# Kernel optimization log

Measured on AMD Instinct MI355X. Metric: run time of the kernel, lower is better.

The kernel has to match this reference:

```python
import jax, jax.numpy as jnp
import numpy as np

D_MODEL = 1024
N_HEADS = 16
HEAD_DIM = D_MODEL // N_HEADS
FFN_DIM = 4096
T = 2048
LN_EPS = 1e-5


def layer_norm(x, g, b):
    mu = jnp.mean(x, axis=-1, keepdims=True)
    var = jnp.mean(jnp.square(x - mu), axis=-1, keepdims=True)
    return (x - mu) * jax.lax.rsqrt(var + LN_EPS) * g + b


def setup_inputs() -> dict:
    key = jax.random.key(0)
    ks = jax.random.split(key, 12)
    s = 0.02
    x = jax.random.normal(ks[0], (1, T, D_MODEL), dtype=jnp.float32)
    # causal mask: True means masked (strict upper triangle)
    causal_mask = jnp.triu(jnp.ones((T, T), dtype=bool), k=1)
    # ALiBi bias: -slope * distance, per head
    slopes = 2.0 ** (-8.0 * (jnp.arange(1, N_HEADS + 1, dtype=jnp.float32) / N_HEADS))
    pos = jnp.arange(T, dtype=jnp.float32)
    dist = pos[None, :] - pos[:, None]  # (T, T)
    alibi_bias = slopes[:, None, None] * jnp.minimum(dist, 0.0)[None]  # (H, T, T)
    inp = {
        "x": x,
        "causal_mask": causal_mask,
        "alibi_bias": alibi_bias.astype(jnp.float32),
        "wq": jax.random.normal(ks[1], (D_MODEL, D_MODEL), jnp.float32) * s,
        "bq": jnp.zeros((D_MODEL,), jnp.float32),
        "wk": jax.random.normal(ks[2], (D_MODEL, D_MODEL), jnp.float32) * s,
        "bk": jnp.zeros((D_MODEL,), jnp.float32),
        "wv": jax.random.normal(ks[3], (D_MODEL, D_MODEL), jnp.float32) * s,
        "bv": jnp.zeros((D_MODEL,), jnp.float32),
        "wo": jax.random.normal(ks[4], (D_MODEL, D_MODEL), jnp.float32) * s,
        "bo": jnp.zeros((D_MODEL,), jnp.float32),
        "w1": jax.random.normal(ks[5], (D_MODEL, FFN_DIM), jnp.float32) * s,
        "b1": jnp.zeros((FFN_DIM,), jnp.float32),
        "w2": jax.random.normal(ks[6], (FFN_DIM, D_MODEL), jnp.float32) * s,
        "b2": jnp.zeros((D_MODEL,), jnp.float32),
        "g1": jnp.ones((D_MODEL,), jnp.float32),
        "be1": jnp.zeros((D_MODEL,), jnp.float32),
        "g2": jnp.ones((D_MODEL,), jnp.float32),
        "be2": jnp.zeros((D_MODEL,), jnp.float32),
    }
    return inp


def reference(x, causal_mask, alibi_bias, wq, bq, wk, bk, wv, bv, wo, bo,
              w1, b1, w2, b2, g1, be1, g2, be2):
    B, Tt, D = x.shape
    H, hd = N_HEADS, HEAD_DIM
    x_norm = layer_norm(x, g1, be1)
    # projections -> (B, H, T, hd)
    def split_heads(y):
        return y.reshape(B, Tt, H, hd).transpose(0, 2, 1, 3)
    Q = split_heads(x_norm @ wq + bq)
    K = split_heads(x_norm @ wk + bk)
    V = split_heads(x_norm @ wv + bv)
    scale = jnp.sqrt(jnp.float32(hd))
    scores = jnp.einsum('bhqd,bhkd->bhqk', Q, K) / scale
    scores = scores + alibi_bias[None]
    scores = jnp.where(causal_mask[None, None], -jnp.inf, scores)
    attn = jax.nn.softmax(scores, axis=-1)
    attn_out = jnp.einsum('bhqk,bhkd->bhqd', attn, V)
    attn_out = attn_out.transpose(0, 2, 1, 3).reshape(B, Tt, D)
    attn_out = attn_out @ wo + bo
    x = x + attn_out
    x_norm = layer_norm(x, g2, be2)
    h = jax.nn.gelu(x_norm @ w1 + b1, approximate=False)
    ffn_out = h @ w2 + b2
    return x + ffn_out
```

## Files before the change

kernel.cpp:

```cpp
#include <hip/hip_runtime.h>
#include <hip/hip_bf16.h>
#include <math.h>

#define T_SEQ 2048
#define D_MODEL 1024
#define N_HEADS 16
#define HEAD_DIM 64
#define FFN_DIM 4096

typedef _Float16 halfx8 __attribute__((ext_vector_type(8)));
typedef _Float16 halfx4 __attribute__((ext_vector_type(4)));
typedef float floatx4 __attribute__((ext_vector_type(4)));

__device__ __forceinline__ void async_ld16(const _Float16* g, _Float16* l) {
  __builtin_amdgcn_global_load_lds(
      (const __attribute__((address_space(1))) unsigned int*)g,
      (__attribute__((address_space(3))) unsigned int*)l, 16, 0, 0);
}

template <int N> __device__ __forceinline__ void wait_barrier();
template <> __device__ __forceinline__ void wait_barrier<3>() {
  asm volatile("s_waitcnt vmcnt(3)\n\ts_barrier" ::: "memory");
}
template <> __device__ __forceinline__ void wait_barrier<4>() {
  asm volatile("s_waitcnt vmcnt(4)\n\ts_barrier" ::: "memory");
}

__global__ __launch_bounds__(256) void ln_h_kernel(
    const float* __restrict__ x, const float* __restrict__ g,
    const float* __restrict__ b, _Float16* __restrict__ y) {
  int row = blockIdx.x;
  const float* xr = x + (size_t)row * D_MODEL;
  _Float16* yr = y + (size_t)row * D_MODEL;
  int tid = threadIdx.x;
  int lid = tid & 63, wid = tid >> 6;
  __shared__ float red[8];

  float4 v = *(const float4*)&xr[tid * 4];
  float sum = v.x + v.y + v.z + v.w;
  for (int o = 32; o > 0; o >>= 1) sum += __shfl_down(sum, o, 64);
  if (lid == 0) red[wid] = sum;
  __syncthreads();
  if (tid == 0) { float t = 0; for (int i = 0; i < 4; i++) t += red[i]; red[0] = t; }
  __syncthreads();
  float mu = red[0] * (1.0f / D_MODEL);
  __syncthreads();

  float dx = v.x - mu, dy = v.y - mu, dz = v.z - mu, dw = v.w - mu;
  float vs = dx * dx + dy * dy + dz * dz + dw * dw;
  for (int o = 32; o > 0; o >>= 1) vs += __shfl_down(vs, o, 64);
  if (lid == 0) red[wid] = vs;
  __syncthreads();
  if (tid == 0) { float t = 0; for (int i = 0; i < 4; i++) t += red[i]; red[0] = t; }
  __syncthreads();
  float rstd = rsqrtf(red[0] * (1.0f / D_MODEL) + 1e-5f);

  float4 gv = *(const float4*)&g[tid * 4];
  float4 bv = *(const float4*)&b[tid * 4];
  halfx4 o;
  o[0] = (_Float16)(dx * rstd * gv.x + bv.x);
  o[1] = (_Float16)(dy * rstd * gv.y + bv.y);
  o[2] = (_Float16)(dz * rstd * gv.z + bv.z);
  o[3] = (_Float16)(dw * rstd * gv.w + bv.w);
  *(halfx4*)&yr[tid * 4] = o;
}

__global__ __launch_bounds__(256) void prep_kernel(
    const float* __restrict__ wq, const float* __restrict__ wk,
    const float* __restrict__ wv, const float* __restrict__ wo,
    const float* __restrict__ w1, const float* __restrict__ w2,
    const float* __restrict__ bq, const float* __restrict__ bk,
    const float* __restrict__ bv, _Float16* __restrict__ Wqkvt,
    _Float16* __restrict__ Wot, _Float16* __restrict__ W1t,
    _Float16* __restrict__ W2t, float* __restrict__ bqkv) {
  int bId = blockIdx.x;
  int tid = threadIdx.x;
  if (bId >= 12288) {
    int i = (bId - 12288) * 256 + tid;
    if (i < 1024) bqkv[i] = bq[i];
    else if (i < 2048) bqkv[i] = bk[i - 1024];
    else bqkv[i] = bv[i - 2048];
    return;
  }
  const float* in; _Float16* outp; int K, N, t;
  if (bId < 1024)      { in = wq; outp = Wqkvt;                 K = 1024; N = 1024; t = bId; }
  else if (bId < 2048) { in = wk; outp = Wqkvt + 1024 * 1024;   K = 1024; N = 1024; t = bId - 1024; }
  else if (bId < 3072) { in = wv; outp = Wqkvt + 2 * 1024 * 1024; K = 1024; N = 1024; t = bId - 2048; }
  else if (bId < 4096) { in = wo; outp = Wot;                   K = 1024; N = 1024; t = bId - 3072; }
  else if (bId < 8192) { in = w1; outp = W1t;                   K = 1024; N = 4096; t = bId - 4096; }
  else                 { in = w2; outp = W2t;                   K = 4096; N = 1024; t = bId - 8192; }
  int ntn = N / 32;
  int tk = (t / ntn) * 32, tn = (t % ntn) * 32;

  __shared__ float tile[32][33];
  int r = tid >> 3, c = (tid & 7) * 4;
  float4 v = *(const float4*)&in[(size_t)(tk + r) * N + tn + c];
  tile[r][c] = v.x; tile[r][c + 1] = v.y; tile[r][c + 2] = v.z; tile[r][c + 3] = v.w;
  __syncthreads();
  halfx4 o;
  o[0] = (_Float16)tile[c][r];
  o[1] = (_Float16)tile[c + 1][r];
  o[2] = (_Float16)tile[c + 2][r];
  o[3] = (_Float16)tile[c + 3][r];
  *(halfx4*)&outp[(size_t)(tn + r) * K + tk + c] = o;
}

template <int MODE, int BM, int BN>
__global__ __launch_bounds__(256) void hgemm_kernel(
    const _Float16* __restrict__ A, const _Float16* __restrict__ Bt,
    const float* __restrict__ bias, const float* __restrict__ res,
    float* __restrict__ Cf, _Float16* __restrict__ Ch,
    _Float16* __restrict__ Vtg, int M, int N, int K) {
  constexpr int TM = BM / 32;
  constexpr int TN = BN / 32;
  constexpr int AR = BM / 64;
  constexpr int BR = BN / 64;
  constexpr int L = AR + BR;
  __shared__ _Float16 As[3][BM][32];
  __shared__ _Float16 Bs[3][BN][32];
  const int tid = threadIdx.x;
  const int w = tid >> 6, lane = tid & 63;
  const int l16 = lane & 15, quad = lane >> 4;
  const int m0 = blockIdx.y * BM, n0 = blockIdx.x * BN;
  const int wm = (w >> 1) * (BM / 2), wn = (w & 1) * (BN / 2);

  floatx4 acc[TM][TN];
#pragma unroll
  for (int i = 0; i < TM; i++)
#pragma unroll
    for (int j = 0; j < TN; j++) acc[i][j] = (floatx4){0.f, 0.f, 0.f, 0.f};

  const int srow = w * 16 + (lane >> 2);
  const int gg = (lane & 3) ^ ((srow >> 1) & 3);
  const _Float16* Agp = A + (size_t)(m0 + srow) * K + gg * 8;
  const _Float16* Bgp = Bt + (size_t)(n0 + srow) * K + gg * 8;

  const int colA = (quad ^ ((l16 >> 1) & 3)) * 8;

  const int NIT = K / 32;
#define HG_ISSUE(buf, k0)                                                     \
  {                                                                           \
    _Pragma("unroll") for (int i = 0; i < AR; i++)                            \
        async_ld16(Agp + (k0) + (size_t)i * 64 * K, &As[buf][i * 64 + w * 16][0]); \
    _Pragma("unroll") for (int i = 0; i < BR; i++)                            \
        async_ld16(Bgp + (k0) + (size_t)i * 64 * K, &Bs[buf][i * 64 + w * 16][0]); \
  }
  HG_ISSUE(0, 0)
  if (NIT > 1) HG_ISSUE(1, 32)

  for (int it = 0; it < NIT; it++) {
    const int buf = it % 3;
    wait_barrier<L>();
    if (it + 2 < NIT) HG_ISSUE((it + 2) % 3, (it + 2) * 32)
    halfx8 af[TM], bf[TN];
#pragma unroll
    for (int mt = 0; mt < TM; mt++)
      af[mt] = *(const halfx8*)&As[buf][wm + mt * 16 + l16][colA];
#pragma unroll
    for (int nt = 0; nt < TN; nt++)
      bf[nt] = *(const halfx8*)&Bs[buf][wn + nt * 16 + l16][colA];
#pragma unroll
    for (int mt = 0; mt < TM; mt++)
#pragma unroll
      for (int nt = 0; nt < TN; nt++)
        acc[mt][nt] = __builtin_amdgcn_mfma_f32_16x16x32_f16(af[mt], bf[nt], acc[mt][nt], 0, 0, 0);
  }

#pragma unroll
  for (int mt = 0; mt < TM; mt++) {
    int row0 = m0 + wm + mt * 16 + quad * 4;
#pragma unroll
    for (int nt = 0; nt < TN; nt++) {
      int col = n0 + wn + nt * 16 + l16;
      float bv = bias[col];
      float vv[4];
#pragma unroll
      for (int r = 0; r < 4; r++) {
        float v = acc[mt][nt][r] + bv;
        if (MODE == 1) v = 0.5f * v * (1.0f + erff(v * 0.70710678118f));
        vv[r] = v;
      }
      if (MODE == 2) {
#pragma unroll
        for (int r = 0; r < 4; r++)
          Cf[(size_t)(row0 + r) * N + col] = vv[r] + res[(size_t)(row0 + r) * N + col];
      } else if (MODE == 3) {
        if (col < 2048) {
#pragma unroll
          for (int r = 0; r < 4; r++)
            Ch[(size_t)(row0 + r) * 2048 + col] = (_Float16)vv[r];
        } else {
          halfx4 pk;
#pragma unroll
          for (int r = 0; r < 4; r++) pk[r] = (_Float16)vv[r];
          *(halfx4*)&Vtg[(size_t)(col - 2048) * T_SEQ + row0] = pk;
        }
      } else {
#pragma unroll
        for (int r = 0; r < 4; r++)
          Ch[(size_t)(row0 + r) * N + col] = (_Float16)vv[r];
      }
    }
  }
}

#define LROW 72
__global__ __launch_bounds__(256) void flash_attn_kernel(
    const _Float16* __restrict__ QK, const _Float16* __restrict__ Vtg,
    _Float16* __restrict__ out) {
  __shared__ _Float16 Ks[3][64][64];
  __shared__ _Float16 Vt[3][64][64];
  __shared__ _Float16 Ps[4][16][LROW];

  const int h = blockIdx.y;
  const int qt = 31 - blockIdx.x;
  const int q0 = qt * 64;
  const int tid = threadIdx.x;
  const int w = tid >> 6;
  const int lane = tid & 63;
  const int l16 = lane & 15;
  const int quad = lane >> 4;

  const _Float16* Qg = QK + h * HEAD_DIM;
  const _Float16* Kg = QK + 1024 + h * HEAD_DIM;
  const _Float16* Vg = Vtg + (size_t)h * HEAD_DIM * T_SEQ;

  const _Float16* qp = Qg + (size_t)(q0 + w * 16 + l16) * 2048;
  halfx8 qa0 = *(const halfx8*)(qp + quad * 8);
  halfx8 qa1 = *(const halfx8*)(qp + 32 + quad * 8);

  float m_i[4], l_i[4];
  floatx4 o_acc[4];
#pragma unroll
  for (int r = 0; r < 4; r++) { m_i[r] = -INFINITY; l_i[r] = 0.f; }
#pragma unroll
  for (int c = 0; c < 4; c++) o_acc[c] = (floatx4){0.f, 0.f, 0.f, 0.f};

  const float scale2 = 0.18033688f;
  const float slope2 = exp2f(-0.5f * (float)(h + 1)) * 1.44269504f;
  const int row_base = q0 + w * 16 + quad * 4;

  const int sr = w * 8 + (lane >> 3);
  const int gg = (lane & 7) ^ ((lane >> 3) & 7);
  const _Float16* Kp = Kg + (size_t)sr * 2048 + gg * 8;
  const _Float16* Vp = Vg + (size_t)sr * 2048 + gg * 8;

  const int m7 = l16 & 7;
  const int cK0 = (quad ^ m7) * 8;
  const int cK1 = cK0 ^ 32;
  const int cV0 = (quad ^ m7) * 8;
  const int cV1 = ((quad + 4) ^ m7) * 8;

#define FA_ISSUE(buf, k0)                                                      \
  {                                                                            \
    async_ld16(Kp + (size_t)(k0) * 2048, &Ks[buf][w * 8][0]);                  \
    async_ld16(Kp + (size_t)((k0) + 32) * 2048, &Ks[buf][32 + w * 8][0]);      \
    async_ld16(Vp + (k0), &Vt[buf][w * 8][0]);                                 \
    async_ld16(Vp + (size_t)32 * 2048 + (k0), &Vt[buf][32 + w * 8][0]);        \
  }
  FA_ISSUE(0, 0)
  if (qt >= 1) FA_ISSUE(1, 64)

  for (int t = 0; t <= qt; t++) {
    const int k0 = t * 64;
    const int buf = t % 3;
    wait_barrier<4>();
    if (t + 2 <= qt) FA_ISSUE((t + 2) % 3, (t + 2) * 64)

    float sc[4][4];
#pragma unroll
    for (int sub = 0; sub < 4; sub++) {
      const _Float16* kr = &Ks[buf][sub * 16 + l16][0];
      halfx8 b0 = *(const halfx8*)(kr + cK0);
      halfx8 b1 = *(const halfx8*)(kr + cK1);
      floatx4 acc = (floatx4){0.f, 0.f, 0.f, 0.f};
      acc = __builtin_amdgcn_mfma_f32_16x16x32_f16(qa0, b0, acc, 0, 0, 0);
      acc = __builtin_amdgcn_mfma_f32_16x16x32_f16(qa1, b1, acc, 0, 0, 0);
#pragma unroll
      for (int r = 0; r < 4; r++) sc[sub][r] = acc[r];
    }

    const bool diag = (t == qt);
#pragma unroll
    for (int r = 0; r < 4; r++) {
      const int rg = row_base + r;
      float mx = m_i[r];
#pragma unroll
      for (int sub = 0; sub < 4; sub++) {
        int cg = k0 + sub * 16 + l16;
        float s = sc[sub][r] * scale2 + slope2 * (float)(cg - rg);
        if (diag && cg > rg) s = -1e30f;
        sc[sub][r] = s;
        mx = fmaxf(mx, s);
      }
      mx = fmaxf(mx, __shfl_xor(mx, 1, 64));
      mx = fmaxf(mx, __shfl_xor(mx, 2, 64));
      mx = fmaxf(mx, __shfl_xor(mx, 4, 64));
      mx = fmaxf(mx, __shfl_xor(mx, 8, 64));
      float alpha = exp2f(m_i[r] - mx);
      m_i[r] = mx;
      float ls = 0.f;
#pragma unroll
      for (int sub = 0; sub < 4; sub++) {
        float p = exp2f(sc[sub][r] - mx);
        ls += p;
        Ps[w][quad * 4 + r][sub * 16 + l16] = (_Float16)p;
      }
      ls += __shfl_xor(ls, 1, 64);
      ls += __shfl_xor(ls, 2, 64);
      ls += __shfl_xor(ls, 4, 64);
      ls += __shfl_xor(ls, 8, 64);
      l_i[r] = l_i[r] * alpha + ls;
#pragma unroll
      for (int c = 0; c < 4; c++) o_acc[c][r] *= alpha;
    }

#pragma unroll
    for (int kh = 0; kh < 2; kh++) {
      halfx8 pa = *(const halfx8*)(&Ps[w][l16][kh * 32 + quad * 8]);
      const int cV = kh ? cV1 : cV0;
#pragma unroll
      for (int c = 0; c < 4; c++) {
        halfx8 vb = *(const halfx8*)(&Vt[buf][c * 16 + l16][cV]);
        o_acc[c] = __builtin_amdgcn_mfma_f32_16x16x32_f16(pa, vb, o_acc[c], 0, 0, 0);
      }
    }
  }

#pragma unroll
  for (int c = 0; c < 4; c++)
#pragma unroll
    for (int r = 0; r < 4; r++)
      out[(size_t)(row_base + r) * D_MODEL + h * HEAD_DIM + c * 16 + l16] =
          (_Float16)(o_acc[c][r] / l_i[r]);
}

extern "C" void kernel_launch(void* const* d_in, const int* in_sizes, int n_in,
                              void* d_out, int out_size, void* d_ws, size_t ws_size,
                              hipStream_t stream) {
  const float* x   = (const float*)d_in[0];
  const float* wq  = (const float*)d_in[3];
  const float* bq  = (const float*)d_in[4];
  const float* wk  = (const float*)d_in[5];
  const float* bk  = (const float*)d_in[6];
  const float* wv  = (const float*)d_in[7];
  const float* bv  = (const float*)d_in[8];
  const float* wo  = (const float*)d_in[9];
  const float* bo  = (const float*)d_in[10];
  const float* w1  = (const float*)d_in[11];
  const float* b1  = (const float*)d_in[12];
  const float* w2  = (const float*)d_in[13];
  const float* b2  = (const float*)d_in[14];
  const float* g1  = (const float*)d_in[15];
  const float* be1 = (const float*)d_in[16];
  const float* g2  = (const float*)d_in[17];
  const float* be2 = (const float*)d_in[18];
  float* out = (float*)d_out;

  const size_t TD = (size_t)T_SEQ * D_MODEL;
  char* p = (char*)d_ws;
  float*    x1    = (float*)p;     p += TD * 4;
  float*    bqkv  = (float*)p;     p += 4096 * 4;
  _Float16* xnh   = (_Float16*)p;  p += TD * 2;
  _Float16* QKh   = (_Float16*)p;  p += (size_t)2048 * 2048 * 2;
  _Float16* Vtg   = (_Float16*)p;  p += (size_t)1024 * 2048 * 2;
  _Float16* attnh = (_Float16*)p;  p += TD * 2;
  _Float16* hh    = (_Float16*)p;  p += (size_t)2048 * 4096 * 2;
  _Float16* Wqkvt = (_Float16*)p;  p += (size_t)3 * 1024 * 1024 * 2;
  _Float16* Wot   = (_Float16*)p;  p += (size_t)1024 * 1024 * 2;
  _Float16* W1t   = (_Float16*)p;  p += (size_t)1024 * 4096 * 2;
  _Float16* W2t   = (_Float16*)p;  p += (size_t)4096 * 1024 * 2;

  dim3 blk(256);

  prep_kernel<<<dim3(12300), blk, 0, stream>>>(wq, wk, wv, wo, w1, w2, bq, bk, bv,
                                               Wqkvt, Wot, W1t, W2t, bqkv);

  ln_h_kernel<<<T_SEQ, blk, 0, stream>>>(x, g1, be1, xnh);

  hgemm_kernel<3, 128, 128><<<dim3(3072 / 128, T_SEQ / 128), blk, 0, stream>>>(
      xnh, Wqkvt, bqkv, nullptr, nullptr, QKh, Vtg, T_SEQ, 3072, 1024);

  flash_attn_kernel<<<dim3(T_SEQ / 64, N_HEADS), blk, 0, stream>>>(QKh, Vtg, attnh);

  hgemm_kernel<2, 64, 128><<<dim3(1024 / 128, T_SEQ / 64), blk, 0, stream>>>(
      attnh, Wot, bo, x, x1, nullptr, nullptr, T_SEQ, 1024, 1024);

  ln_h_kernel<<<T_SEQ, blk, 0, stream>>>(x1, g2, be2, xnh);

  hgemm_kernel<1, 128, 128><<<dim3(4096 / 128, T_SEQ / 128), blk, 0, stream>>>(
      xnh, W1t, b1, nullptr, nullptr, hh, nullptr, T_SEQ, 4096, 1024);

  hgemm_kernel<2, 64, 128><<<dim3(1024 / 128, T_SEQ / 64), blk, 0, stream>>>(
      hh, W2t, b2, x1, out, nullptr, nullptr, T_SEQ, 1024, 4096);
}
```

Measured before the change: 584.9 us.

## Fuse weight prep with first LayerNorm, retune GEMM tiles, restructure flash softmax

Merges the weight-transpose prep kernel and the first LayerNorm into a single launch, which removes one kernel launch. Switches the output-projection and FFN2 GEMMs from 64x128 to 64x64 tiles to put more blocks on the GPU. Changes the GEMM tail to drain all outstanding loads on the last iteration. In flash attention, the K/V staging drops from triple to double buffering with a full vmcnt(0) wait each step, and the per-row max/sum shuffles are batched across the four rows to expose more instruction-level parallelism. The shallower attention pipeline may expose load latency that the old triple buffer hid.

Result: faster. 572.3 us (-2.2%).

```diff
diff --git a/kernel.cpp b/kernel.cpp
--- a/kernel.cpp
+++ b/kernel.cpp
@@ -19,11 +19,92 @@
 }
 
 template <int N> __device__ __forceinline__ void wait_barrier();
+template <> __device__ __forceinline__ void wait_barrier<0>() {
+  asm volatile("s_waitcnt vmcnt(0)\n\ts_barrier" ::: "memory");
+}
+template <> __device__ __forceinline__ void wait_barrier<2>() {
+  asm volatile("s_waitcnt vmcnt(2)\n\ts_barrier" ::: "memory");
+}
 template <> __device__ __forceinline__ void wait_barrier<3>() {
   asm volatile("s_waitcnt vmcnt(3)\n\ts_barrier" ::: "memory");
 }
 template <> __device__ __forceinline__ void wait_barrier<4>() {
   asm volatile("s_waitcnt vmcnt(4)\n\ts_barrier" ::: "memory");
+}
+
+__global__ __launch_bounds__(256) void prep_ln_kernel(
+    const float* __restrict__ wq, const float* __restrict__ wk,
+    const float* __restrict__ wv, const float* __restrict__ wo,
+    const float* __restrict__ w1, const float* __restrict__ w2,
+    const float* __restrict__ bq, const float* __restrict__ bk,
+    const float* __restrict__ bv, _Float16* __restrict__ Wqkvt,
+    _Float16* __restrict__ Wot, _Float16* __restrict__ W1t,
+    _Float16* __restrict__ W2t, float* __restrict__ bqkv,
+    const float* __restrict__ x, const float* __restrict__ g1,
+    const float* __restrict__ be1, _Float16* __restrict__ xnh) {
+  int bId = blockIdx.x;
+  int tid = threadIdx.x;
+  if (bId >= 12300) {
+    int row = bId - 12300;
+    const float* xr = x + (size_t)row * D_MODEL;
+    _Float16* yr = xnh + (size_t)row * D_MODEL;
+    int lid = tid & 63, wid = tid >> 6;
+    __shared__ float red[8];
+    float4 v = *(const float4*)&xr[tid * 4];
+    float sum = v.x + v.y + v.z + v.w;
+    for (int o = 32; o > 0; o >>= 1) sum += __shfl_down(sum, o, 64);
+    if (lid == 0) red[wid] = sum;
+    __syncthreads();
+    if (tid == 0) { float t = 0; for (int i = 0; i < 4; i++) t += red[i]; red[0] = t; }
+    __syncthreads();
+    float mu = red[0] * (1.0f / D_MODEL);
+    __syncthreads();
+    float dx = v.x - mu, dy = v.y - mu, dz = v.z - mu, dw = v.w - mu;
+    float vs = dx * dx + dy * dy + dz * dz + dw * dw;
+    for (int o = 32; o > 0; o >>= 1) vs += __shfl_down(vs, o, 64);
+    if (lid == 0) red[wid] = vs;
+    __syncthreads();
+    if (tid == 0) { float t = 0; for (int i = 0; i < 4; i++) t += red[i]; red[0] = t; }
+    __syncthreads();
+    float rstd = rsqrtf(red[0] * (1.0f / D_MODEL) + 1e-5f);
+    float4 gv = *(const float4*)&g1[tid * 4];
+    float4 bv4 = *(const float4*)&be1[tid * 4];
+    halfx4 o;
+    o[0] = (_Float16)(dx * rstd * gv.x + bv4.x);
+    o[1] = (_Float16)(dy * rstd * gv.y + bv4.y);
+    o[2] = (_Float16)(dz * rstd * gv.z + bv4.z);
+    o[3] = (_Float16)(dw * rstd * gv.w + bv4.w);
+    *(halfx4*)&yr[tid * 4] = o;
+    return;
+  }
+  if (bId >= 12288) {
+    int i = (bId - 12288) * 256 + tid;
+    if (i < 1024) bqkv[i] = bq[i];
+    else if (i < 2048) bqkv[i] = bk[i - 1024];
+    else bqkv[i] = bv[i - 2048];
+    return;
+  }
+  const float* in; _Float16* outp; int K, N, t;
+  if (bId < 1024)      { in = wq; outp = Wqkvt;                 K = 1024; N = 1024; t = bId; }
+  else if (bId < 2048) { in = wk; outp = Wqkvt + 1024 * 1024;   K = 1024; N = 1024; t = bId - 1024; }
+  else if (bId < 3072) { in = wv; outp = Wqkvt + 2 * 1024 * 1024; K = 1024; N = 1024; t = bId - 2048; }
+  else if (bId < 4096) { in = wo; outp = Wot;                   K = 1024; N = 1024; t = bId - 3072; }
+  else if (bId < 8192) { in = w1; outp = W1t;                   K = 1024; N = 4096; t = bId - 4096; }
+  else                 { in = w2; outp = W2t;                   K = 4096; N = 1024; t = bId - 8192; }
+  int ntn = N / 32;
+  int tk = (t / ntn) * 32, tn = (t % ntn) * 32;
+
+  __shared__ float tile[32][33];
+  int r = tid >> 3, c = (tid & 7) * 4;
+  float4 v = *(const float4*)&in[(size_t)(tk + r) * N + tn + c];
+  tile[r][c] = v.x; tile[r][c + 1] = v.y; tile[r][c + 2] = v.z; tile[r][c + 3] = v.w;
+  __syncthreads();
+  halfx4 o;
+  o[0] = (_Float16)tile[c][r];
+  o[1] = (_Float16)tile[c + 1][r];
+  o[2] = (_Float16)tile[c + 2][r];
+  o[3] = (_Float16)tile[c + 3][r];
+  *(halfx4*)&outp[(size_t)(tn + r) * K + tk + c] = o;
 }
 
 __global__ __launch_bounds__(256) void ln_h_kernel(
@@ -63,46 +144,6 @@
   o[2] = (_Float16)(dz * rstd * gv.z + bv.z);
   o[3] = (_Float16)(dw * rstd * gv.w + bv.w);
   *(halfx4*)&yr[tid * 4] = o;
-}
-
-__global__ __launch_bounds__(256) void prep_kernel(
-    const float* __restrict__ wq, const float* __restrict__ wk,
-    const float* __restrict__ wv, const float* __restrict__ wo,
-    const float* __restrict__ w1, const float* __restrict__ w2,
-    const float* __restrict__ bq, const float* __restrict__ bk,
-    const float* __restrict__ bv, _Float16* __restrict__ Wqkvt,
-    _Float16* __restrict__ Wot, _Float16* __restrict__ W1t,
-    _Float16* __restrict__ W2t, float* __restrict__ bqkv) {
-  int bId = blockIdx.x;
-  int tid = threadIdx.x;
-  if (bId >= 12288) {
-    int i = (bId - 12288) * 256 + tid;
-    if (i < 1024) bqkv[i] = bq[i];
-    else if (i < 2048) bqkv[i] = bk[i - 1024];
-    else bqkv[i] = bv[i - 2048];
-    return;
-  }
-  const float* in; _Float16* outp; int K, N, t;
-  if (bId < 1024)      { in = wq; outp = Wqkvt;                 K = 1024; N = 1024; t = bId; }
-  else if (bId < 2048) { in = wk; outp = Wqkvt + 1024 * 1024;   K = 1024; N = 1024; t = bId - 1024; }
-  else if (bId < 3072) { in = wv; outp = Wqkvt + 2 * 1024 * 1024; K = 1024; N = 1024; t = bId - 2048; }
-  else if (bId < 4096) { in = wo; outp = Wot;                   K = 1024; N = 1024; t = bId - 3072; }
-  else if (bId < 8192) { in = w1; outp = W1t;                   K = 1024; N = 4096; t = bId - 4096; }
-  else                 { in = w2; outp = W2t;                   K = 4096; N = 1024; t = bId - 8192; }
-  int ntn = N / 32;
-  int tk = (t / ntn) * 32, tn = (t % ntn) * 32;
-
-  __shared__ float tile[32][33];
-  int r = tid >> 3, c = (tid & 7) * 4;
-  float4 v = *(const float4*)&in[(size_t)(tk + r) * N + tn + c];
-  tile[r][c] = v.x; tile[r][c + 1] = v.y; tile[r][c + 2] = v.z; tile[r][c + 3] = v.w;
-  __syncthreads();
-  halfx4 o;
-  o[0] = (_Float16)tile[c][r];
-  o[1] = (_Float16)tile[c + 1][r];
-  o[2] = (_Float16)tile[c + 2][r];
-  o[3] = (_Float16)tile[c + 3][r];
-  *(halfx4*)&outp[(size_t)(tn + r) * K + tk + c] = o;
 }
 
 template <int MODE, int BM, int BN>
@@ -146,11 +187,12 @@
         async_ld16(Bgp + (k0) + (size_t)i * 64 * K, &Bs[buf][i * 64 + w * 16][0]); \
   }
   HG_ISSUE(0, 0)
-  if (NIT > 1) HG_ISSUE(1, 32)
+  HG_ISSUE(1, 32)
 
   for (int it = 0; it < NIT; it++) {
     const int buf = it % 3;
-    wait_barrier<L>();
+    if (it + 1 < NIT) wait_barrier<L>();
+    else wait_barrier<0>();
     if (it + 2 < NIT) HG_ISSUE((it + 2) % 3, (it + 2) * 32)
     halfx8 af[TM], bf[TN];
 #pragma unroll
@@ -208,8 +250,8 @@
 __global__ __launch_bounds__(256) void flash_attn_kernel(
     const _Float16* __restrict__ QK, const _Float16* __restrict__ Vtg,
     _Float16* __restrict__ out) {
-  __shared__ _Float16 Ks[3][64][64];
-  __shared__ _Float16 Vt[3][64][64];
+  __shared__ _Float16 Ks[2][64][64];
+  __shared__ _Float16 Vt[2][64][64];
   __shared__ _Float16 Ps[4][16][LROW];
 
   const int h = blockIdx.y;
@@ -229,13 +271,6 @@
   halfx8 qa0 = *(const halfx8*)(qp + quad * 8);
   halfx8 qa1 = *(const halfx8*)(qp + 32 + quad * 8);
 
-  float m_i[4], l_i[4];
-  floatx4 o_acc[4];
-#pragma unroll
-  for (int r = 0; r < 4; r++) { m_i[r] = -INFINITY; l_i[r] = 0.f; }
-#pragma unroll
-  for (int c = 0; c < 4; c++) o_acc[c] = (floatx4){0.f, 0.f, 0.f, 0.f};
-
   const float scale2 = 0.18033688f;
   const float slope2 = exp2f(-0.5f * (float)(h + 1)) * 1.44269504f;
   const int row_base = q0 + w * 16 + quad * 4;
@@ -258,14 +293,21 @@
     async_ld16(Vp + (k0), &Vt[buf][w * 8][0]);                                 \
     async_ld16(Vp + (size_t)32 * 2048 + (k0), &Vt[buf][32 + w * 8][0]);        \
   }
+
+  float m_i[4], l_i[4];
+  floatx4 o_acc[4];
+#pragma unroll
+  for (int r = 0; r < 4; r++) { m_i[r] = -INFINITY; l_i[r] = 0.f; }
+#pragma unroll
+  for (int c = 0; c < 4; c++) o_acc[c] = (floatx4){0.f, 0.f, 0.f, 0.f};
+
   FA_ISSUE(0, 0)
-  if (qt >= 1) FA_ISSUE(1, 64)
 
   for (int t = 0; t <= qt; t++) {
     const int k0 = t * 64;
-    const int buf = t % 3;
-    wait_barrier<4>();
-    if (t + 2 <= qt) FA_ISSUE((t + 2) % 3, (t + 2) * 64)
+    const int buf = t & 1;
+    wait_barrier<0>();
+    if (t < qt) FA_ISSUE(buf ^ 1, k0 + 64)
 
     float sc[4][4];
 #pragma unroll
@@ -281,38 +323,48 @@
     }
 
     const bool diag = (t == qt);
+    float mx[4];
 #pragma unroll
     for (int r = 0; r < 4; r++) {
       const int rg = row_base + r;
-      float mx = m_i[r];
+      float ab = slope2 * (float)(k0 + l16 - rg);
+      mx[r] = m_i[r];
 #pragma unroll
       for (int sub = 0; sub < 4; sub++) {
-        int cg = k0 + sub * 16 + l16;
-        float s = sc[sub][r] * scale2 + slope2 * (float)(cg - rg);
-        if (diag && cg > rg) s = -1e30f;
+        float s = sc[sub][r] * scale2 + (ab + slope2 * (float)(sub * 16));
+        if (diag && (k0 + sub * 16 + l16) > rg) s = -1e30f;
         sc[sub][r] = s;
-        mx = fmaxf(mx, s);
+        mx[r] = fmaxf(mx[r], s);
       }
-      mx = fmaxf(mx, __shfl_xor(mx, 1, 64));
-      mx = fmaxf(mx, __shfl_xor(mx, 2, 64));
-      mx = fmaxf(mx, __shfl_xor(mx, 4, 64));
-      mx = fmaxf(mx, __shfl_xor(mx, 8, 64));
-      float alpha = exp2f(m_i[r] - mx);
-      m_i[r] = mx;
-      float ls = 0.f;
+    }
+#pragma unroll
+    for (int st = 1; st <= 8; st <<= 1)
+#pragma unroll
+      for (int r = 0; r < 4; r++) mx[r] = fmaxf(mx[r], __shfl_xor(mx[r], st, 64));
+
+    float ls[4], alpha[4];
+#pragma unroll
+    for (int r = 0; r < 4; r++) {
+      alpha[r] = exp2f(m_i[r] - mx[r]);
+      m_i[r] = mx[r];
+      float l = 0.f;
 #pragma unroll
       for (int sub = 0; sub < 4; sub++) {
-        float p = exp2f(sc[sub][r] - mx);
-        ls += p;
+        float p = exp2f(sc[sub][r] - mx[r]);
+        l += p;
         Ps[w][quad * 4 + r][sub * 16 + l16] = (_Float16)p;
       }
-      ls += __shfl_xor(ls, 1, 64);
-      ls += __shfl_xor(ls, 2, 64);
-      ls += __shfl_xor(ls, 4, 64);
-      ls += __shfl_xor(ls, 8, 64);
-      l_i[r] = l_i[r] * alpha + ls;
-#pragma unroll
-      for (int c = 0; c < 4; c++) o_acc[c][r] *= alpha;
+      ls[r] = l;
+    }
+#pragma unroll
+    for (int st = 1; st <= 8; st <<= 1)
+#pragma unroll
+      for (int r = 0; r < 4; r++) ls[r] += __shfl_xor(ls[r], st, 64);
+#pragma unroll
+    for (int r = 0; r < 4; r++) {
+      l_i[r] = l_i[r] * alpha[r] + ls[r];
+#pragma unroll
+      for (int c = 0; c < 4; c++) o_acc[c][r] *= alpha[r];
     }
 
 #pragma unroll
@@ -373,17 +425,16 @@
 
   dim3 blk(256);
 
-  prep_kernel<<<dim3(12300), blk, 0, stream>>>(wq, wk, wv, wo, w1, w2, bq, bk, bv,
-                                               Wqkvt, Wot, W1t, W2t, bqkv);
-
-  ln_h_kernel<<<T_SEQ, blk, 0, stream>>>(x, g1, be1, xnh);
+  prep_ln_kernel<<<dim3(12300 + T_SEQ), blk, 0, stream>>>(
+      wq, wk, wv, wo, w1, w2, bq, bk, bv, Wqkvt, Wot, W1t, W2t, bqkv,
+      x, g1, be1, xnh);
 
   hgemm_kernel<3, 128, 128><<<dim3(3072 / 128, T_SEQ / 128), blk, 0, stream>>>(
       xnh, Wqkvt, bqkv, nullptr, nullptr, QKh, Vtg, T_SEQ, 3072, 1024);
 
   flash_attn_kernel<<<dim3(T_SEQ / 64, N_HEADS), blk, 0, stream>>>(QKh, Vtg, attnh);
 
-  hgemm_kernel<2, 64, 128><<<dim3(1024 / 128, T_SEQ / 64), blk, 0, stream>>>(
+  hgemm_kernel<2, 64, 64><<<dim3(1024 / 64, T_SEQ / 64), blk, 0, stream>>>(
       attnh, Wot, bo, x, x1, nullptr, nullptr, T_SEQ, 1024, 1024);
 
   ln_h_kernel<<<T_SEQ, blk, 0, stream>>>(x1, g2, be2, xnh);
@@ -391,6 +442,6 @@
   hgemm_kernel<1, 128, 128><<<dim3(4096 / 128, T_SEQ / 128), blk, 0, stream>>>(
       xnh, W1t, b1, nullptr, nullptr, hh, nullptr, T_SEQ, 4096, 1024);
 
-  hgemm_kernel<2, 64, 128><<<dim3(1024 / 128, T_SEQ / 64), blk, 0, stream>>>(
+  hgemm_kernel<2, 64, 64><<<dim3(1024 / 64, T_SEQ / 64), blk, 0, stream>>>(
       hh, W2t, b2, x1, out, nullptr, nullptr, T_SEQ, 1024, 4096);
 }
```
